# Kernel tuning notes

Measured on AMD Instinct MI355X. Metric: run time of the kernel, lower is better.

Reference implementation:

```python
import jax, jax.numpy as jnp
import numpy as np

MERSENNE_P = (1 << 31) - 1  # prime used by universal hashing


def _uhash_cols(random_numbers, n_full_cols, n_comp_cols):
    """Universal-hash map from full-weight column index -> compressed column index.
    h(j) = ((r0*j + r1) mod P) mod n_comp_cols  (ints stay well within int64).
    """
    j = jnp.arange(n_full_cols, dtype=jnp.int64)
    r0 = random_numbers[0]
    r1 = random_numbers[1]
    return ((r0 * j + r1) % MERSENNE_P) % n_comp_cols


def setup_inputs() -> dict:
    key = jax.random.key(0)
    k1, k2, k3 = jax.random.split(key, 3)
    in_features, out_features, redn_factor = 8192, 8192, 4
    init_scale = 1.0 / np.sqrt(in_features)
    x = jax.random.normal(k1, (64, in_features), dtype=jnp.float32)
    weight = jax.random.uniform(
        k2, (out_features, in_features // redn_factor), dtype=jnp.float32,
        minval=-init_scale, maxval=init_scale)
    random_numbers = jax.random.randint(k3, (4,), 1, 1048576, dtype=jnp.int64)
    return {"x": x, "weight": weight, "random_numbers": random_numbers,
            "redn_factor": 4}


def reference(x, weight, random_numbers, redn_factor):
    # x: [..., K]; weight (compressed): [N, K // redn_factor]
    orig_shape = x.shape
    K = orig_shape[-1]
    x2d = x.reshape(-1, K)                      # preprocess: flatten leading dims
    n_comp = weight.shape[1]
    col_idx = _uhash_cols(random_numbers, K, n_comp)   # [K] hashed gather indices
    w_full = weight[:, col_idx]                 # [N, K] expanded via hashed gather
    y = x2d @ w_full.T                          # [rows, N]
    return y.reshape(*orig_shape[:-1], y.shape[-1])  # postprocess
```

## Files before the change

### kernel.cpp

```cpp
#include <hip/hip_runtime.h>

#define K_FULL   8192
#define M_ROWS   64
#define N_OUT    8192
#define N_COMP   2048
#define P_MERS   2147483647


typedef __attribute__((ext_vector_type(8))) short bf16x8;
typedef __attribute__((ext_vector_type(4))) float f32x4;

__device__ __forceinline__ unsigned short f2bf(float f) {
    unsigned int u = __float_as_uint(f);
    unsigned int r = (u + 0x7FFFu + ((u >> 16) & 1u)) >> 16;
    return (unsigned short)r;
}

__device__ __forceinline__ int hash_col(int j, int rn0, int rn1, int rn2, int rn3) {
    if (rn1 == 0 && rn3 == 0) {
        long long r0 = (long long)rn0;
        long long r1 = (long long)rn2;
        long long h = (r0 * (long long)j + r1) % (long long)P_MERS;
        return (int)(h % (long long)N_COMP);
    } else {
        unsigned int t = (unsigned int)rn0 * (unsigned int)j + (unsigned int)rn1;
        int ti = (int)t;
        int m1 = ti % P_MERS;
        if (m1 < 0) m1 += P_MERS;
        return m1 & (N_COMP - 1);
    }
}

__global__ __launch_bounds__(512) void k_part(const float* __restrict__ x,
                                              const int* __restrict__ rn,
                                              float* __restrict__ partial) {
    __shared__ float row[N_COMP];
    const int b = blockIdx.x;
    const int m = b >> 2;
    const int jq = b & 3;
    const int tid = threadIdx.x;
#pragma unroll
    for (int i = 0; i < 4; ++i) row[tid + 512 * i] = 0.0f;
    const int rn0 = rn[0], rn1 = rn[1], rn2 = rn[2], rn3 = rn[3];
    __syncthreads();

    const int j0 = jq * 2048 + tid * 4;
    float4 v = *(const float4*)(x + (size_t)m * K_FULL + j0);
    atomicAdd(&row[hash_col(j0 + 0, rn0, rn1, rn2, rn3)], v.x);
    atomicAdd(&row[hash_col(j0 + 1, rn0, rn1, rn2, rn3)], v.y);
    atomicAdd(&row[hash_col(j0 + 2, rn0, rn1, rn2, rn3)], v.z);
    atomicAdd(&row[hash_col(j0 + 3, rn0, rn1, rn2, rn3)], v.w);
    __syncthreads();

    float4 o = { row[4 * tid], row[4 * tid + 1], row[4 * tid + 2], row[4 * tid + 3] };
    *(float4*)(partial + (size_t)b * N_COMP + 4 * tid) = o;
}

__global__ __launch_bounds__(256) void k_pack(const float* __restrict__ partial,
                                              unsigned short* __restrict__ xcB) {
    const int b = blockIdx.x;
    const int m = b >> 2;
    const int c0 = (b & 3) * 512 + threadIdx.x * 2;
    const float* p = partial + (size_t)m * 4 * N_COMP + c0;
    float s0 = p[0] + p[N_COMP] + p[2 * N_COMP] + p[3 * N_COMP];
    float s1 = p[1] + p[N_COMP + 1] + p[2 * N_COMP + 1] + p[3 * N_COMP + 1];
    unsigned int pk = (unsigned int)f2bf(s0) | ((unsigned int)f2bf(s1) << 16);
    ((unsigned int*)(xcB + (size_t)m * N_COMP))[c0 >> 1] = pk;
}

#define KSLICES 4
#define KSL     (N_COMP / KSLICES)
#define KSTEPS  (KSL / 32)

__global__ __launch_bounds__(256) void k_gemm(const float* __restrict__ W,
                                              const unsigned short* __restrict__ xcB,
                                              float* __restrict__ y) {
    __shared__ float ys[KSLICES][M_ROWS][16];
    const int tid  = threadIdx.x;
    const int lane = tid & 63;
    const int w    = __builtin_amdgcn_readfirstlane(tid >> 6);
    const int nr   = lane & 15;
    const int kg   = lane >> 4;
    const int n0   = blockIdx.x * 16;

    const float*          wp = W   + (size_t)(n0 + nr) * N_COMP + w * KSL + kg * 8;
    const unsigned short* ap = xcB + (size_t)nr * N_COMP        + w * KSL + kg * 8;

    f32x4 acc0 = {0.f, 0.f, 0.f, 0.f};
    f32x4 acc1 = {0.f, 0.f, 0.f, 0.f};
    f32x4 acc2 = {0.f, 0.f, 0.f, 0.f};
    f32x4 acc3 = {0.f, 0.f, 0.f, 0.f};

#define LOADW(W0, W1, S) do { int ko_ = (S) * 32;                      \
        (W0) = *(const float4*)(wp + ko_);                             \
        (W1) = *(const float4*)(wp + ko_ + 4); } while (0)
#define LOADA(A0, A1, A2, A3, S) do { int ko_ = (S) * 32;              \
        (A0) = *(const bf16x8*)(ap + ko_);                             \
        (A1) = *(const bf16x8*)(ap + 16 * N_COMP + ko_);               \
        (A2) = *(const bf16x8*)(ap + 32 * N_COMP + ko_);               \
        (A3) = *(const bf16x8*)(ap + 48 * N_COMP + ko_); } while (0)
#define DOMFMA(W0, W1, A0, A1, A2, A3) do { bf16x8 b_;                 \
        b_[0] = (short)f2bf((W0).x); b_[1] = (short)f2bf((W0).y);      \
        b_[2] = (short)f2bf((W0).z); b_[3] = (short)f2bf((W0).w);      \
        b_[4] = (short)f2bf((W1).x); b_[5] = (short)f2bf((W1).y);      \
        b_[6] = (short)f2bf((W1).z); b_[7] = (short)f2bf((W1).w);      \
        acc0 = __builtin_amdgcn_mfma_f32_16x16x32_bf16((A0), b_, acc0, 0, 0, 0); \
        acc1 = __builtin_amdgcn_mfma_f32_16x16x32_bf16((A1), b_, acc1, 0, 0, 0); \
        acc2 = __builtin_amdgcn_mfma_f32_16x16x32_bf16((A2), b_, acc2, 0, 0, 0); \
        acc3 = __builtin_amdgcn_mfma_f32_16x16x32_bf16((A3), b_, acc3, 0, 0, 0); } while (0)

    float4 wa0, wa1, wb0, wb1;
    bf16x8 aa0, aa1, aa2, aa3, ab0, ab1, ab2, ab3;

    LOADW(wa0, wa1, 0);
    LOADA(aa0, aa1, aa2, aa3, 0);
#pragma unroll 1
    for (int s = 0; s < KSTEPS - 2; s += 2) {
        LOADW(wb0, wb1, s + 1);
        LOADA(ab0, ab1, ab2, ab3, s + 1);
        DOMFMA(wa0, wa1, aa0, aa1, aa2, aa3);
        LOADW(wa0, wa1, s + 2);
        LOADA(aa0, aa1, aa2, aa3, s + 2);
        DOMFMA(wb0, wb1, ab0, ab1, ab2, ab3);
    }
    LOADW(wb0, wb1, KSTEPS - 1);
    LOADA(ab0, ab1, ab2, ab3, KSTEPS - 1);
    DOMFMA(wa0, wa1, aa0, aa1, aa2, aa3);
    DOMFMA(wb0, wb1, ab0, ab1, ab2, ab3);

#pragma unroll
    for (int j = 0; j < 4; ++j) {
        ys[w][ 0 + kg * 4 + j][nr] = acc0[j];
        ys[w][16 + kg * 4 + j][nr] = acc1[j];
        ys[w][32 + kg * 4 + j][nr] = acc2[j];
        ys[w][48 + kg * 4 + j][nr] = acc3[j];
    }
    __syncthreads();

#pragma unroll
    for (int i = 0; i < 4; ++i) {
        int o = tid + 256 * i;
        int m = o >> 4;
        int n = o & 15;
        float s = ys[0][m][n] + ys[1][m][n] + ys[2][m][n] + ys[3][m][n];
        y[(size_t)m * N_OUT + n0 + n] = s;
    }
}

extern "C" void kernel_launch(void* const* d_in, const int* in_sizes, int n_in,
                              void* d_out, int out_size, void* d_ws, size_t ws_size,
                              hipStream_t stream) {
    const float* x = (const float*)d_in[0];
    const float* W = (const float*)d_in[1];
    const int* rn  = (const int*)d_in[2];
    float* y       = (float*)d_out;

    float* partial      = (float*)d_ws;
    unsigned short* xcB = (unsigned short*)((char*)d_ws + 256 * N_COMP * sizeof(float));

    k_part<<<256, 512, 0, stream>>>(x, rn, partial);
    k_pack<<<256, 256, 0, stream>>>(partial, xcB);
    k_gemm<<<N_OUT / 16, 256, 0, stream>>>(W, xcB, y);
}
```

Before: 36.34 us.

## Split GEMM K across eight waves, use Mersenne reduction hash and intrinsic bf16 conversion

The GEMM kernel now splits the compressed K dimension into eight slices handled by eight waves (512 threads per block) instead of four. The goal is more memory-level parallelism per block while streaming the 64 MB fp32 weight. The 64-bit modulo in the hash is replaced by a Mersenne-prime fold, and the manual bf16 rounding is swapped for the HIP intrinsic conversion. In exchange, the per-block shared memory for the partial-sum reduction doubles, and the epilogue sums eight partials instead of four.

Measured after the change: 36.24 us. About the same (-0.3%).

```diff
diff --git a/kernel.cpp b/kernel.cpp
--- a/kernel.cpp
+++ b/kernel.cpp
@@ -1,4 +1,5 @@
 #include <hip/hip_runtime.h>
+#include <hip/hip_bf16.h>
 
 #define K_FULL   8192
 #define M_ROWS   64
@@ -10,18 +11,18 @@
 typedef __attribute__((ext_vector_type(8))) short bf16x8;
 typedef __attribute__((ext_vector_type(4))) float f32x4;
 
-__device__ __forceinline__ unsigned short f2bf(float f) {
-    unsigned int u = __float_as_uint(f);
-    unsigned int r = (u + 0x7FFFu + ((u >> 16) & 1u)) >> 16;
-    return (unsigned short)r;
+__device__ __forceinline__ short f2bfs(float f) {
+    __hip_bfloat16 h = __float2bfloat16(f);
+    return *reinterpret_cast<short*>(&h);
 }
 
 __device__ __forceinline__ int hash_col(int j, int rn0, int rn1, int rn2, int rn3) {
     if (rn1 == 0 && rn3 == 0) {
-        long long r0 = (long long)rn0;
-        long long r1 = (long long)rn2;
-        long long h = (r0 * (long long)j + r1) % (long long)P_MERS;
-        return (int)(h % (long long)N_COMP);
+        unsigned long long xx = (unsigned long long)(unsigned int)rn0 * (unsigned int)j
+                              + (unsigned long long)(unsigned int)rn2;
+        unsigned long long t = (xx & (unsigned long long)P_MERS) + (xx >> 31);
+        if (t >= (unsigned long long)P_MERS) t -= (unsigned long long)P_MERS;
+        return (int)(t & (N_COMP - 1));
     } else {
         unsigned int t = (unsigned int)rn0 * (unsigned int)j + (unsigned int)rn1;
         int ti = (int)t;
@@ -64,15 +65,16 @@
     const float* p = partial + (size_t)m * 4 * N_COMP + c0;
     float s0 = p[0] + p[N_COMP] + p[2 * N_COMP] + p[3 * N_COMP];
     float s1 = p[1] + p[N_COMP + 1] + p[2 * N_COMP + 1] + p[3 * N_COMP + 1];
-    unsigned int pk = (unsigned int)f2bf(s0) | ((unsigned int)f2bf(s1) << 16);
+    unsigned int pk = (unsigned int)(unsigned short)f2bfs(s0)
+                    | ((unsigned int)(unsigned short)f2bfs(s1) << 16);
     ((unsigned int*)(xcB + (size_t)m * N_COMP))[c0 >> 1] = pk;
 }
 
-#define KSLICES 4
+#define KSLICES 8
 #define KSL     (N_COMP / KSLICES)
 #define KSTEPS  (KSL / 32)
 
-__global__ __launch_bounds__(256) void k_gemm(const float* __restrict__ W,
+__global__ __launch_bounds__(512) void k_gemm(const float* __restrict__ W,
                                               const unsigned short* __restrict__ xcB,
                                               float* __restrict__ y) {
     __shared__ float ys[KSLICES][M_ROWS][16];
@@ -100,10 +102,10 @@
         (A2) = *(const bf16x8*)(ap + 32 * N_COMP + ko_);               \
         (A3) = *(const bf16x8*)(ap + 48 * N_COMP + ko_); } while (0)
 #define DOMFMA(W0, W1, A0, A1, A2, A3) do { bf16x8 b_;                 \
-        b_[0] = (short)f2bf((W0).x); b_[1] = (short)f2bf((W0).y);      \
-        b_[2] = (short)f2bf((W0).z); b_[3] = (short)f2bf((W0).w);      \
-        b_[4] = (short)f2bf((W1).x); b_[5] = (short)f2bf((W1).y);      \
-        b_[6] = (short)f2bf((W1).z); b_[7] = (short)f2bf((W1).w);      \
+        b_[0] = f2bfs((W0).x); b_[1] = f2bfs((W0).y);                  \
+        b_[2] = f2bfs((W0).z); b_[3] = f2bfs((W0).w);                  \
+        b_[4] = f2bfs((W1).x); b_[5] = f2bfs((W1).y);                  \
+        b_[6] = f2bfs((W1).z); b_[7] = f2bfs((W1).w);                  \
         acc0 = __builtin_amdgcn_mfma_f32_16x16x32_bf16((A0), b_, acc0, 0, 0, 0); \
         acc1 = __builtin_amdgcn_mfma_f32_16x16x32_bf16((A1), b_, acc1, 0, 0, 0); \
         acc2 = __builtin_amdgcn_mfma_f32_16x16x32_bf16((A2), b_, acc2, 0, 0, 0); \
@@ -138,11 +140,13 @@
     __syncthreads();
 
 #pragma unroll
-    for (int i = 0; i < 4; ++i) {
-        int o = tid + 256 * i;
+    for (int i = 0; i < 2; ++i) {
+        int o = tid + 512 * i;
         int m = o >> 4;
         int n = o & 15;
-        float s = ys[0][m][n] + ys[1][m][n] + ys[2][m][n] + ys[3][m][n];
+        float s = 0.f;
+#pragma unroll
+        for (int q = 0; q < KSLICES; ++q) s += ys[q][m][n];
         y[(size_t)m * N_OUT + n0 + n] = s;
     }
 }
@@ -160,5 +164,5 @@
 
     k_part<<<256, 512, 0, stream>>>(x, rn, partial);
     k_pack<<<256, 256, 0, stream>>>(partial, xcB);
-    k_gemm<<<N_OUT / 16, 256, 0, stream>>>(W, xcB, y);
+    k_gemm<<<N_OUT / 16, 512, 0, stream>>>(W, xcB, y);
 }
```
